# Optimization experiments

Measured on AMD Instinct MI355X. Metric: run time of the kernel, lower is better.

Reference implementation:

```python
import jax, jax.numpy as jnp
import numpy as np

ALPHA = 0.2  # LeakyReLU negative slope

def setup_inputs() -> dict:
    key = jax.random.key(0)
    k1, k2, k3 = jax.random.split(key, 3)
    B, N, Fin, Fout = 8, 2048, 256, 128
    h = jax.random.normal(k1, (B, N, Fin), dtype=jnp.float32)
    W = jax.random.normal(k2, (Fin, Fout), dtype=jnp.float32) * (1.414 / np.sqrt(Fin))
    a = jax.random.normal(k3, (2 * Fout, 1), dtype=jnp.float32) * 0.1
    return {"h": h, "W": W, "a": a}

def reference(h, W, a):
    # Wh: [B, N, D]
    Wh = jnp.einsum('bni,io->bno', h, W)
    D = Wh.shape[-1]
    a1 = a[:D, 0]   # weights for the 'i' (repeat_interleave) half
    a2 = a[D:, 0]   # weights for the 'j' (repeat) half
    s1 = Wh @ a1    # [B, N]
    s2 = Wh @ a2    # [B, N]
    # e[b,i,j] = leakyrelu(s1[b,i] + s2[b,j])  (fused form of the O(N^2*2D) concat)
    e = s1[:, :, None] + s2[:, None, :]
    e = jnp.where(e >= 0, e, ALPHA * e)
    # original applies softmax over dim=1 (the i axis)
    attention = jax.nn.softmax(e, axis=1)
    # dropout is identity in eval mode
    h_prime = jnp.einsum('bij,bjd->bid', attention, Wh)
    # concat=True -> ELU
    return jax.nn.elu(h_prime)
```

## Files before the change

kernel.cpp:

```cpp
#include <hip/hip_runtime.h>
#include <hip/hip_bf16.h>


#define ALPHA 0.2f
#define LOG2E 1.4426950408889634f
constexpr int Bb=8, Nn=2048, FIN=256, FOUT=128;

typedef __attribute__((ext_vector_type(8))) short short8;
typedef __attribute__((ext_vector_type(4))) float f32x4;
typedef __attribute__((ext_vector_type(16))) float f32x16;
typedef const __attribute__((address_space(1))) unsigned int* gptr_t;
typedef __attribute__((address_space(3))) unsigned int* lptr_t;

__device__ __forceinline__ float lrelu(float x){ return fmaxf(x, ALPHA*x); }
__device__ __forceinline__ unsigned short bfbits(float x){
    __hip_bfloat16 h = __float2bfloat16(x);
    return *(unsigned short*)&h;
}

__global__ __launch_bounds__(256) void k_prep(const float* __restrict__ W,
                                              __hip_bfloat16* __restrict__ WTt){
    const int idx = blockIdx.x*256 + threadIdx.x;
    #pragma unroll
    for (int v = 0; v < 4; ++v){
        const int widx = idx + v*8192;
        const int kk = widx & 31, n = (widx>>5)&127, kt = widx>>12;
        WTt[widx] = __float2bfloat16(W[(kt*32+kk)*FOUT + n]);
    }
}

__global__ __launch_bounds__(256) void k_wh(const float* __restrict__ h,
                                            const float* __restrict__ a,
                                            const __hip_bfloat16* __restrict__ WTt,
                                            float* __restrict__ s1,
                                            float* __restrict__ s2,
                                            __hip_bfloat16* __restrict__ WhT){
    const int blk = blockIdx.x;
    const int rowbase = blk * 32;
    const int b = blk >> 6;
    const int jt = (rowbase & (Nn-1)) >> 5;
    const int t = threadIdx.x;
    const int wave = t>>6, lane = t&63;
    const int wm = wave & 1, wn = wave >> 1;
    const int lm = lane & 15, q = lane >> 4;

    __shared__ __align__(16) float hs[32*260];
    __shared__ unsigned short tt[FOUT*40];
    __shared__ float s1red[2][32], s2red[2][32];

    {
        const float* srcbase = h + (size_t)rowbase*FIN;
        #pragma unroll
        for (int c = 0; c < 8; ++c){
            const int row = wave*8 + c;
            __builtin_amdgcn_global_load_lds(
                (gptr_t)(srcbase + (size_t)row*FIN + lane*4),
                (lptr_t)&hs[row*260], 16, 0, 0);
        }
    }
    __syncthreads();

    f32x4 acc[4];
    #pragma unroll
    for (int ntl = 0; ntl < 4; ++ntl) acc[ntl] = (f32x4){0.f,0.f,0.f,0.f};

    const float* hrow = &hs[(wm*16 + lm)*260];
    const short* Wt = (const short*)WTt;
    #pragma unroll
    for (int kt = 0; kt < 8; ++kt){
        float av[8];
        *(float4*)&av[0] = *(const float4*)&hrow[kt*32 + q*8];
        *(float4*)&av[4] = *(const float4*)&hrow[kt*32 + q*8 + 4];
        short8 afr;
        #pragma unroll
        for (int e = 0; e < 8; ++e) afr[e] = (short)bfbits(av[e]);
        #pragma unroll
        for (int ntl = 0; ntl < 4; ++ntl){
            const short8 bfr = *(const short8*)(Wt + ((kt*128 + wn*64 + ntl*16 + lm)*32 + q*8));
            acc[ntl] = __builtin_amdgcn_mfma_f32_16x16x32_bf16(afr, bfr, acc[ntl], 0,0,0);
        }
    }

    {
        float a1v[4], a2v[4];
        #pragma unroll
        for (int ntl = 0; ntl < 4; ++ntl){
            a1v[ntl] = a[wn*64 + ntl*16 + lm];
            a2v[ntl] = a[FOUT + wn*64 + ntl*16 + lm];
        }
        #pragma unroll
        for (int rg = 0; rg < 4; ++rg){
            float p1 = 0.f, p2 = 0.f;
            #pragma unroll
            for (int ntl = 0; ntl < 4; ++ntl){
                p1 += acc[ntl][rg]*a1v[ntl];
                p2 += acc[ntl][rg]*a2v[ntl];
            }
            #pragma unroll
            for (int m = 1; m < 16; m <<= 1){
                p1 += __shfl_xor(p1, m);
                p2 += __shfl_xor(p2, m);
            }
            if (lm == 0){
                s1red[wn][wm*16 + q*4 + rg] = p1;
                s2red[wn][wm*16 + q*4 + rg] = p2;
            }
        }
    }

    #pragma unroll
    for (int ntl = 0; ntl < 4; ++ntl){
        ushort4 u;
        u.x = bfbits(acc[ntl][0]); u.y = bfbits(acc[ntl][1]);
        u.z = bfbits(acc[ntl][2]); u.w = bfbits(acc[ntl][3]);
        *(ushort4*)&tt[(wn*64 + ntl*16 + lm)*40 + wm*16 + q*4] = u;
    }
    __syncthreads();

    if (t < 32){
        s1[rowbase + t] = (s1red[0][t] + s1red[1][t]) * LOG2E;
        s2[rowbase + t] = (s2red[0][t] + s2red[1][t]) * LOG2E;
    }
    {
        const int d = t >> 1, jsub16 = t & 1;
        const unsigned short* src = &tt[d*40 + jsub16*16];
        short8 v0 = *(const short8*)src;
        short8 v1 = *(const short8*)(src + 8);
        const int s  = (jt & 1)*2 + jsub16;
        const int nt = d >> 5, col = d & 31;
        const int u0 = (s*4 + nt)*64 + col;
        short* Wo = (short*)WhT;
        const size_t tb = ((size_t)(b*32 + (jt >> 1)))*8192;
        *(short8*)&Wo[tb + (size_t)u0*8]      = v0;
        *(short8*)&Wo[tb + (size_t)(u0+32)*8] = v1;
    }
}

__global__ __launch_bounds__(256) void k_z(const float* __restrict__ s1,
                                           const float* __restrict__ s2,
                                           float* __restrict__ Aout,
                                           float* __restrict__ Bout){
    const int b  = blockIdx.x >> 6;
    const int jt = blockIdx.x & 63;
    const int t  = threadIdx.x;
    const int jj = t & 31, part = t >> 5;
    const int j  = jt*32 + jj;
    __shared__ float s1s[Nn];
    __shared__ float red[8][33];

    {
        const float4* g = (const float4*)(s1 + (size_t)b*Nn);
        float4* p = (float4*)s1s;
        #pragma unroll
        for (int v0 = 0; v0 < 2; ++v0){ const int v = t + v0*256; p[v] = g[v]; }
    }
    __syncthreads();
    const float s2j = s2[b*Nn + j];
    float sum = 0.f;
    const float4* s4 = (const float4*)&s1s[part*256];
    #pragma unroll 4
    for (int v = 0; v < 64; ++v){
        float x[4]; *(float4*)x = s4[v];
        sum += __builtin_amdgcn_exp2f(lrelu(x[0]+s2j))
             + __builtin_amdgcn_exp2f(lrelu(x[1]+s2j))
             + __builtin_amdgcn_exp2f(lrelu(x[2]+s2j))
             + __builtin_amdgcn_exp2f(lrelu(x[3]+s2j));
    }
    red[part][jj] = sum;
    __syncthreads();
    if (part == 0){
        float Z = 0.f;
        #pragma unroll
        for (int p = 0; p < 8; ++p) Z += red[p][jj];
        const float lz = -__builtin_amdgcn_logf(Z);
        Aout[b*Nn + j] = s2j + lz;
        Bout[b*Nn + j] = ALPHA*s2j + lz;
    }
}

__global__ __launch_bounds__(512) void k_pv(const float* __restrict__ s1,
                                            const float* __restrict__ Aarr,
                                            const float* __restrict__ Barr,
                                            const __hip_bfloat16* __restrict__ WhT,
                                            float* __restrict__ out){
    const int blk   = blockIdx.x;
    const int b     = blk & 7;
    const int ibase = (blk >> 3) * 64;
    const int t     = threadIdx.x;
    const int wave  = t >> 6, lane = t & 63;
    const int wr = wave & 1, kh = wave >> 1;
    const int il = lane & 31, l5 = lane >> 5;

    __shared__ __align__(16) float comb[4*32*132];

    const float s1a  = s1[(size_t)b*Nn + ibase + wr*32 + il];
    const float as1a = ALPHA * s1a;
    const float* Ab = Aarr + (size_t)b*Nn;
    const float* Zb = Barr + (size_t)b*Nn;

    f32x16 acc[4];
    #pragma unroll
    for (int nt = 0; nt < 4; ++nt)
        #pragma unroll
        for (int e = 0; e < 16; ++e) acc[nt][e] = 0.f;

    const char* Wtb = (const char*)WhT + (size_t)b*32*16384;

    for (int it = 0; it < 8; ++it){
        const char* tile = Wtb + (size_t)(kh*8 + it)*16384;
        #pragma unroll
        for (int s = 0; s < 4; ++s){
            short8 bfr[4];
            #pragma unroll
            for (int nt = 0; nt < 4; ++nt)
                bfr[nt] = *(const short8*)(tile + (size_t)(((s*4 + nt)*64 + lane)*16));

            const int jb = kh*512 + it*64 + s*16 + l5*8;
            float av[8], bv[8];
            *(float4*)&av[0] = *(const float4*)&Ab[jb];
            *(float4*)&av[4] = *(const float4*)&Ab[jb+4];
            *(float4*)&bv[0] = *(const float4*)&Zb[jb];
            *(float4*)&bv[4] = *(const float4*)&Zb[jb+4];
            short8 afa;
            #pragma unroll
            for (int e = 0; e < 8; ++e)
                afa[e] = (short)bfbits(__builtin_amdgcn_exp2f(
                             fmaxf(s1a + av[e], as1a + bv[e])));
            #pragma unroll
            for (int nt = 0; nt < 4; ++nt)
                acc[nt] = __builtin_amdgcn_mfma_f32_32x32x16_bf16(afa, bfr[nt], acc[nt], 0,0,0);
        }
    }

    __syncthreads();
    if (kh < 2){
        float* cb = comb + (size_t)(kh*2 + wr)*(32*132);
        #pragma unroll
        for (int nt = 0; nt < 4; ++nt)
            #pragma unroll
            for (int r = 0; r < 16; ++r){
                const int row = (r&3) + 8*(r>>2) + 4*l5;
                cb[row*132 + nt*32 + il] = acc[nt][r];
            }
    }
    __syncthreads();
    if (kh >= 2){
        float* cb = comb + (size_t)((kh-2)*2 + wr)*(32*132);
        #pragma unroll
        for (int nt = 0; nt < 4; ++nt)
            #pragma unroll
            for (int r = 0; r < 16; ++r){
                const int row = (r&3) + 8*(r>>2) + 4*l5;
                cb[row*132 + nt*32 + il] += acc[nt][r];
            }
    }
    __syncthreads();
    {
        const int rgrp = t >> 5, c4 = (t & 31)*4;
        #pragma unroll
        for (int rr = 0; rr < 4; ++rr){
            const int row = rgrp*4 + rr;
            const int wrr = row >> 5, rin = row & 31;
            const float* r0 = comb + (size_t)(wrr)*(32*132)       + rin*132 + c4;
            const float* r1 = comb + (size_t)(2 + wrr)*(32*132)   + rin*132 + c4;
            float4 v0 = *(const float4*)r0, v1 = *(const float4*)r1;
            float o[4];
            #pragma unroll
            for (int e = 0; e < 4; ++e){
                const float x = ((const float*)&v0)[e] + ((const float*)&v1)[e];
                o[e] = x > 0.f ? x : expm1f(x);
            }
            *(float4*)&out[((size_t)(b*Nn + ibase + row))*FOUT + c4] = *(float4*)o;
        }
    }
}

extern "C" void kernel_launch(void* const* d_in, const int* in_sizes, int n_in,
                              void* d_out, int out_size, void* d_ws, size_t ws_size,
                              hipStream_t stream) {
    (void)in_sizes; (void)n_in; (void)out_size; (void)ws_size;
    const float* h = (const float*)d_in[0];
    const float* W = (const float*)d_in[1];
    const float* a = (const float*)d_in[2];
    float* out = (float*)d_out;

    float* ws    = (float*)d_ws;
    float* s1    = ws;
    float* s2    = s1 + Bb*Nn;
    float* Aarr  = s2 + Bb*Nn;
    float* Barr  = Aarr + Bb*Nn;
    __hip_bfloat16* WTt = (__hip_bfloat16*)(Barr + Bb*Nn);
    __hip_bfloat16* WhT = WTt + 32768;

    k_prep<<<dim3(32),        dim3(256), 0, stream>>>(W, WTt);
    k_wh  <<<dim3(Bb*Nn/32),  dim3(256), 0, stream>>>(h, a, WTt, s1, s2, WhT);
    k_z   <<<dim3(Bb*64),     dim3(256), 0, stream>>>(s1, s2, Aarr, Barr);
    k_pv  <<<dim3(Bb*Nn/64),  dim3(512), 0, stream>>>(s1, Aarr, Barr, WhT, out);
}
```

Measured before the change: 103.5 us.

## Drop W prep kernel, write Wh directly, double-buffer Wh tiles in LDS

Removes the separate W transpose/convert kernel: k_wh now reads fp32 W directly with strided loads and converts it to bf16 in registers. k_wh also skips the LDS transpose staging and writes its bf16 tiles straight to global. k_pv stages each Wh tile into a double-buffered LDS region with async global_load_lds, prefetching the next tile during the MFMA work, and sets launch bounds for two blocks per CU. This trades one launch and some global latency for extra uncoalesced W reads, more redundant conversion, and 128KB of LDS per block, which may not allow the intended occupancy.

```diff
diff --git a/kernel.cpp b/kernel.cpp
--- a/kernel.cpp
+++ b/kernel.cpp
@@ -18,20 +18,9 @@
     return *(unsigned short*)&h;
 }
 
-__global__ __launch_bounds__(256) void k_prep(const float* __restrict__ W,
-                                              __hip_bfloat16* __restrict__ WTt){
-    const int idx = blockIdx.x*256 + threadIdx.x;
-    #pragma unroll
-    for (int v = 0; v < 4; ++v){
-        const int widx = idx + v*8192;
-        const int kk = widx & 31, n = (widx>>5)&127, kt = widx>>12;
-        WTt[widx] = __float2bfloat16(W[(kt*32+kk)*FOUT + n]);
-    }
-}
-
 __global__ __launch_bounds__(256) void k_wh(const float* __restrict__ h,
+                                            const float* __restrict__ W,
                                             const float* __restrict__ a,
-                                            const __hip_bfloat16* __restrict__ WTt,
                                             float* __restrict__ s1,
                                             float* __restrict__ s2,
                                             __hip_bfloat16* __restrict__ WhT){
@@ -45,7 +34,6 @@
     const int lm = lane & 15, q = lane >> 4;
 
     __shared__ __align__(16) float hs[32*260];
-    __shared__ unsigned short tt[FOUT*40];
     __shared__ float s1red[2][32], s2red[2][32];
 
     {
@@ -65,7 +53,7 @@
     for (int ntl = 0; ntl < 4; ++ntl) acc[ntl] = (f32x4){0.f,0.f,0.f,0.f};
 
     const float* hrow = &hs[(wm*16 + lm)*260];
-    const short* Wt = (const short*)WTt;
+    const float* Wq   = W + (size_t)(q*8)*FOUT + wn*64 + lm;
     #pragma unroll
     for (int kt = 0; kt < 8; ++kt){
         float av[8];
@@ -74,9 +62,13 @@
         short8 afr;
         #pragma unroll
         for (int e = 0; e < 8; ++e) afr[e] = (short)bfbits(av[e]);
+        const float* Wkt = Wq + (size_t)kt*32*FOUT;
         #pragma unroll
         for (int ntl = 0; ntl < 4; ++ntl){
-            const short8 bfr = *(const short8*)(Wt + ((kt*128 + wn*64 + ntl*16 + lm)*32 + q*8));
+            const float* Wp = Wkt + ntl*16;
+            short8 bfr;
+            #pragma unroll
+            for (int e = 0; e < 8; ++e) bfr[e] = (short)bfbits(Wp[(size_t)e*FOUT]);
             acc[ntl] = __builtin_amdgcn_mfma_f32_16x16x32_bf16(afr, bfr, acc[ntl], 0,0,0);
         }
     }
@@ -108,31 +100,26 @@
         }
     }
 
-    #pragma unroll
-    for (int ntl = 0; ntl < 4; ++ntl){
-        ushort4 u;
-        u.x = bfbits(acc[ntl][0]); u.y = bfbits(acc[ntl][1]);
-        u.z = bfbits(acc[ntl][2]); u.w = bfbits(acc[ntl][3]);
-        *(ushort4*)&tt[(wn*64 + ntl*16 + lm)*40 + wm*16 + q*4] = u;
-    }
-    __syncthreads();
-
+    {
+        short* Wo = (short*)WhT;
+        const size_t tb = ((size_t)(b*32 + (jt >> 1)))*8192;
+        const int s  = (jt & 1)*2 + wm;
+        const int l5 = q >> 1, ehalf = (q & 1)*4;
+        #pragma unroll
+        for (int ntl = 0; ntl < 4; ++ntl){
+            const int d = wn*64 + ntl*16 + lm;
+            const int u = (s*4 + (d>>5))*64 + l5*32 + (d & 31);
+            ushort4 v;
+            v.x = bfbits(acc[ntl][0]); v.y = bfbits(acc[ntl][1]);
+            v.z = bfbits(acc[ntl][2]); v.w = bfbits(acc[ntl][3]);
+            *(ushort4*)&Wo[tb + (size_t)u*8 + ehalf] = v;
+        }
+    }
+
+    __syncthreads();
     if (t < 32){
         s1[rowbase + t] = (s1red[0][t] + s1red[1][t]) * LOG2E;
         s2[rowbase + t] = (s2red[0][t] + s2red[1][t]) * LOG2E;
-    }
-    {
-        const int d = t >> 1, jsub16 = t & 1;
-        const unsigned short* src = &tt[d*40 + jsub16*16];
-        short8 v0 = *(const short8*)src;
-        short8 v1 = *(const short8*)(src + 8);
-        const int s  = (jt & 1)*2 + jsub16;
-        const int nt = d >> 5, col = d & 31;
-        const int u0 = (s*4 + nt)*64 + col;
-        short* Wo = (short*)WhT;
-        const size_t tb = ((size_t)(b*32 + (jt >> 1)))*8192;
-        *(short8*)&Wo[tb + (size_t)u0*8]      = v0;
-        *(short8*)&Wo[tb + (size_t)(u0+32)*8] = v1;
     }
 }
 
@@ -178,11 +165,11 @@
     }
 }
 
-__global__ __launch_bounds__(512) void k_pv(const float* __restrict__ s1,
-                                            const float* __restrict__ Aarr,
-                                            const float* __restrict__ Barr,
-                                            const __hip_bfloat16* __restrict__ WhT,
-                                            float* __restrict__ out){
+__global__ __launch_bounds__(512, 2) void k_pv(const float* __restrict__ s1,
+                                               const float* __restrict__ Aarr,
+                                               const float* __restrict__ Barr,
+                                               const __hip_bfloat16* __restrict__ WhT,
+                                               float* __restrict__ out){
     const int blk   = blockIdx.x;
     const int b     = blk & 7;
     const int ibase = (blk >> 3) * 64;
@@ -191,7 +178,7 @@
     const int wr = wave & 1, kh = wave >> 1;
     const int il = lane & 31, l5 = lane >> 5;
 
-    __shared__ __align__(16) float comb[4*32*132];
+    __shared__ unsigned short Bs[2][4][8192];
 
     const float s1a  = s1[(size_t)b*Nn + ibase + wr*32 + il];
     const float as1a = ALPHA * s1a;
@@ -205,15 +192,35 @@
         for (int e = 0; e < 16; ++e) acc[nt][e] = 0.f;
 
     const char* Wtb = (const char*)WhT + (size_t)b*32*16384;
-
+    const int laneoff = wr*8192 + lane*16;
+
+    {
+        const char* src = Wtb + (size_t)(kh*8)*16384 + laneoff;
+        unsigned short* dst = &Bs[0][kh][wr*4096];
+        #pragma unroll
+        for (int c = 0; c < 8; ++c)
+            __builtin_amdgcn_global_load_lds((gptr_t)(src + c*1024),
+                                             (lptr_t)(dst + c*512), 16, 0, 0);
+    }
+
+    int buf = 0;
     for (int it = 0; it < 8; ++it){
-        const char* tile = Wtb + (size_t)(kh*8 + it)*16384;
+        __syncthreads();
+        if (it + 1 < 8){
+            const char* src = Wtb + (size_t)(kh*8 + it + 1)*16384 + laneoff;
+            unsigned short* dst = &Bs[buf^1][kh][wr*4096];
+            #pragma unroll
+            for (int c = 0; c < 8; ++c)
+                __builtin_amdgcn_global_load_lds((gptr_t)(src + c*1024),
+                                                 (lptr_t)(dst + c*512), 16, 0, 0);
+        }
+        const char* tile = (const char*)&Bs[buf][kh][0];
         #pragma unroll
         for (int s = 0; s < 4; ++s){
             short8 bfr[4];
             #pragma unroll
             for (int nt = 0; nt < 4; ++nt)
-                bfr[nt] = *(const short8*)(tile + (size_t)(((s*4 + nt)*64 + lane)*16));
+                bfr[nt] = *(const short8*)(tile + ((s*4 + nt)*64 + lane)*16);
 
             const int jb = kh*512 + it*64 + s*16 + l5*8;
             float av[8], bv[8];
@@ -230,9 +237,11 @@
             for (int nt = 0; nt < 4; ++nt)
                 acc[nt] = __builtin_amdgcn_mfma_f32_32x32x16_bf16(afa, bfr[nt], acc[nt], 0,0,0);
         }
-    }
-
-    __syncthreads();
+        buf ^= 1;
+    }
+
+    __syncthreads();
+    float* comb = (float*)&Bs[0][0][0];
     if (kh < 2){
         float* cb = comb + (size_t)(kh*2 + wr)*(32*132);
         #pragma unroll
@@ -289,11 +298,9 @@
     float* s2    = s1 + Bb*Nn;
     float* Aarr  = s2 + Bb*Nn;
     float* Barr  = Aarr + Bb*Nn;
-    __hip_bfloat16* WTt = (__hip_bfloat16*)(Barr + Bb*Nn);
-    __hip_bfloat16* WhT = WTt + 32768;
-
-    k_prep<<<dim3(32),        dim3(256), 0, stream>>>(W, WTt);
-    k_wh  <<<dim3(Bb*Nn/32),  dim3(256), 0, stream>>>(h, a, WTt, s1, s2, WhT);
+    __hip_bfloat16* WhT = (__hip_bfloat16*)(Barr + Bb*Nn);
+
+    k_wh  <<<dim3(Bb*Nn/32),  dim3(256), 0, stream>>>(h, W, a, s1, s2, WhT);
     k_z   <<<dim3(Bb*64),     dim3(256), 0, stream>>>(s1, s2, Aarr, Barr);
     k_pv  <<<dim3(Bb*Nn/64),  dim3(512), 0, stream>>>(s1, Aarr, Barr, WhT, out);
 }
```

Measured after the change: 105.2 us. No clear change (+1.6%).
